# Kernel optimization log

Measured on AMD Instinct MI355X. Metric: run time of the kernel, lower is better.

Reference implementation:

```python
import jax, jax.numpy as jnp
import numpy as np

M, K, N = 8192, 4096, 4096
SCALE_D = 0.05  # per-tensor activation quant step

def setup_inputs() -> dict:
    key = jax.random.key(0)
    k1, k2, k3, k4 = jax.random.split(key, 4)
    x = jax.random.normal(k1, (M, K), jnp.float32)
    # already-quantized int8 weight, stored transposed as in the module: [K, N]
    q_weight = jax.random.randint(k2, (K, N), -127, 128).astype(jnp.int8)
    # per-tensor activation quant: act_scale = 1/scale_d, act_offset = 0
    act_scale = jnp.asarray(1.0 / SCALE_D, jnp.float32)
    act_offset = jnp.asarray(0.0, jnp.float32)
    # per-output-channel weight scales -> deq_scale = scale_d * scale_w, shape [N]
    scale_w = jax.random.uniform(k3, (N,), jnp.float32, 0.001, 0.01)
    deq_scale = (SCALE_D * scale_w).astype(jnp.float32)
    # int32 bias = round(bias_f / (scale_d * scale_w))
    bias_f = jax.random.normal(k4, (N,), jnp.float32) * 0.1
    bias_i32 = jnp.round(bias_f / deq_scale).astype(jnp.int32)
    return {"x": x, "q_weight": q_weight, "act_scale": act_scale,
            "act_offset": act_offset, "deq_scale": deq_scale, "bias_i32": bias_i32}

def reference(x, q_weight, act_scale, act_offset, deq_scale, bias_i32):
    # npu_quantize(div_mode=False): q = clamp(round(x * scale + offset), int8)
    qx = jnp.clip(jnp.round(x * act_scale + act_offset), -128.0, 127.0).astype(jnp.int8)
    # npu_quant_matmul: int8 GEMM accumulated in int32, + int32 bias, * deq_scale
    acc = jnp.matmul(qx.astype(jnp.int32), q_weight.astype(jnp.int32),
                     preferred_element_type=jnp.int32)  # [M, N] int32
    out = (acc + bias_i32[None, :]).astype(jnp.float32) * deq_scale[None, :]
    return out
```

## Files before the change

kernel.cpp:

```cpp
#include <hip/hip_runtime.h>
#include <stdint.h>

#define GM 8192
#define GK 4096
#define GN 4096

typedef int v4i __attribute__((ext_vector_type(4)));

__device__ __forceinline__ void async_load16(const void* gptr, void* lptr) {
  __builtin_amdgcn_global_load_lds(
      (const __attribute__((address_space(1))) void*)gptr,
      (__attribute__((address_space(3))) void*)lptr,
      16 , 0 , 0 );
}

__global__ __launch_bounds__(256) void quant_kernel(
    const float* __restrict__ x, int8_t* __restrict__ qx,
    const float* __restrict__ scale_p, const float* __restrict__ off_p) {
  const int i = blockIdx.x * 256 + threadIdx.x;
  const float s = scale_p[0], o = off_p[0];
  const float4 f = ((const float4*)x)[i];
  float a = fminf(fmaxf(rintf(f.x * s + o), -128.f), 127.f);
  float b = fminf(fmaxf(rintf(f.y * s + o), -128.f), 127.f);
  float c = fminf(fmaxf(rintf(f.z * s + o), -128.f), 127.f);
  float d = fminf(fmaxf(rintf(f.w * s + o), -128.f), 127.f);
  int packed = (((int)a) & 0xff) | ((((int)b) & 0xff) << 8) |
               ((((int)c) & 0xff) << 16) | ((((int)d) & 0xff) << 24);
  ((int*)qx)[i] = packed;
}

__global__ __launch_bounds__(256) void transpose_kernel(
    const int* __restrict__ B, int8_t* __restrict__ Bt) {
  __shared__ int tile32[64][65];
  const int t = threadIdx.x;
  const int n0 = blockIdx.x * 64;
  const int k0 = blockIdx.y * 64;
#pragma unroll
  for (int r = 0; r < 4; ++r) {
    const int kl = r * 16 + (t >> 4);
    const int nl = (t & 15) * 4;
    const int4 v = *(const int4*)(B + (size_t)(k0 + kl) * GN + n0 + nl);
    *(int4*)&tile32[kl][nl] = v;
  }
  __syncthreads();
  const int nl = t >> 2;
  const int kc = (t & 3) * 16;
  v4i out;
#pragma unroll
  for (int w = 0; w < 4; ++w) {
    int p = 0;
#pragma unroll
    for (int j = 0; j < 4; ++j)
      p |= (tile32[kc + w * 4 + j][nl] & 0xff) << (8 * j);
    out[w] = p;
  }
  *(v4i*)(Bt + (size_t)(n0 + nl) * GK + k0 + kc) = out;
}

__global__ __launch_bounds__(256) void gemm_i8_kernel(
    const int8_t* __restrict__ A, const int8_t* __restrict__ Bt,
    const int* __restrict__ bias, const float* __restrict__ deq,
    float* __restrict__ C) {
  __shared__ __align__(16) int8_t Alds[128 * 64];
  __shared__ __align__(16) int8_t Blds[128 * 64];

  const int t = threadIdx.x;
  const int lane = t & 63;
  const int wave = t >> 6;
  const int m0 = blockIdx.y * 128;
  const int n0 = blockIdx.x * 128;
  const int wm = (wave >> 1) * 64;
  const int wn = (wave & 1) * 64;

  v4i acc[4][4];
  const v4i vzero = {0, 0, 0, 0};
#pragma unroll
  for (int mi = 0; mi < 4; ++mi)
#pragma unroll
    for (int ni = 0; ni < 4; ++ni) acc[mi][ni] = vzero;

  const int srow = t >> 2;
  const int scol = (t & 3) * 16;
  const int8_t* ag0 = A + (size_t)(m0 + srow) * GK + scol;
  const int8_t* ag1 = ag0 + (size_t)64 * GK;
  const int8_t* bg0 = Bt + (size_t)(n0 + srow) * GK + scol;
  const int8_t* bg1 = bg0 + (size_t)64 * GK;
  int8_t* al0 = Alds + t * 16;
  int8_t* al1 = al0 + 64 * 64;
  int8_t* bl0 = Blds + t * 16;
  int8_t* bl1 = bl0 + 64 * 64;

  const int fr = lane & 15;
  const int kg = (lane >> 4) * 16;

  for (int k0 = 0; k0 < GK; k0 += 64) {
    __syncthreads();
    async_load16(ag0 + k0, al0);
    async_load16(ag1 + k0, al1);
    async_load16(bg0 + k0, bl0);
    async_load16(bg1 + k0, bl1);
    __syncthreads();

    v4i af[4], bf[4];
#pragma unroll
    for (int i = 0; i < 4; ++i) {
      af[i] = *(const v4i*)(Alds + (size_t)(wm + i * 16 + fr) * 64 + kg);
      bf[i] = *(const v4i*)(Blds + (size_t)(wn + i * 16 + fr) * 64 + kg);
    }
#pragma unroll
    for (int mi = 0; mi < 4; ++mi)
#pragma unroll
      for (int ni = 0; ni < 4; ++ni)
        acc[mi][ni] =
            __builtin_amdgcn_mfma_i32_16x16x64_i8(af[mi], bf[ni], acc[mi][ni], 0, 0, 0);
  }

  const int col = lane & 15;
  const int rq = (lane >> 4) * 4;
#pragma unroll
  for (int ni = 0; ni < 4; ++ni) {
    const int gc = n0 + wn + ni * 16 + col;
    const float d = deq[gc];
    const int bs = bias[gc];
#pragma unroll
    for (int mi = 0; mi < 4; ++mi) {
      const int gr = m0 + wm + mi * 16 + rq;
#pragma unroll
      for (int r = 0; r < 4; ++r)
        C[(size_t)(gr + r) * GN + gc] = (float)(acc[mi][ni][r] + bs) * d;
    }
  }
}

extern "C" void kernel_launch(void* const* d_in, const int* in_sizes, int n_in,
                              void* d_out, int out_size, void* d_ws, size_t ws_size,
                              hipStream_t stream) {
  const float* x = (const float*)d_in[0];
  const int* qw = (const int*)d_in[1];
  const float* act_scale = (const float*)d_in[2];
  const float* act_offset = (const float*)d_in[3];
  const float* deq = (const float*)d_in[4];
  const int* bias = (const int*)d_in[5];
  float* out = (float*)d_out;

  int8_t* qx = (int8_t*)d_ws;
  int8_t* Bt = (int8_t*)d_ws + (size_t)GM * GK;

  const int n4 = GM * GK / 4;
  quant_kernel<<<n4 / 256, 256, 0, stream>>>(x, qx, act_scale, act_offset);
  transpose_kernel<<<dim3(GN / 64, GK / 64), 256, 0, stream>>>(qw, Bt);
  gemm_i8_kernel<<<dim3(GN / 128, GM / 128), 256, 0, stream>>>(qx, Bt, bias, deq, out);
}
```

Before: 422.4 us.

## Fuse quant and transpose launches; process two K-tiles per barrier in int8 GEMM

Quantization and weight transpose are merged into one kernel launch, with block index selecting the job, which removes a launch and lets both jobs run concurrently. The GEMM main loop now loads two 64-wide K slices into two LDS buffers per iteration, halving the number of barrier pairs and increasing outstanding global loads. LDS use doubles to 32KB per block, which may reduce occupancy.

New measurement: 411.3 us. 2.6% less time.

```diff
diff --git a/kernel.cpp b/kernel.cpp
--- a/kernel.cpp
+++ b/kernel.cpp
@@ -14,55 +14,59 @@
       16 , 0 , 0 );
 }
 
-__global__ __launch_bounds__(256) void quant_kernel(
+#define TBLK ((GN / 64) * (GK / 64))
+#define QBLK (GM * GK / 4 / 256)
+
+__global__ __launch_bounds__(256) void prep_kernel(
     const float* __restrict__ x, int8_t* __restrict__ qx,
-    const float* __restrict__ scale_p, const float* __restrict__ off_p) {
-  const int i = blockIdx.x * 256 + threadIdx.x;
-  const float s = scale_p[0], o = off_p[0];
-  const float4 f = ((const float4*)x)[i];
-  float a = fminf(fmaxf(rintf(f.x * s + o), -128.f), 127.f);
-  float b = fminf(fmaxf(rintf(f.y * s + o), -128.f), 127.f);
-  float c = fminf(fmaxf(rintf(f.z * s + o), -128.f), 127.f);
-  float d = fminf(fmaxf(rintf(f.w * s + o), -128.f), 127.f);
-  int packed = (((int)a) & 0xff) | ((((int)b) & 0xff) << 8) |
-               ((((int)c) & 0xff) << 16) | ((((int)d) & 0xff) << 24);
-  ((int*)qx)[i] = packed;
-}
-
-__global__ __launch_bounds__(256) void transpose_kernel(
+    const float* __restrict__ scale_p, const float* __restrict__ off_p,
     const int* __restrict__ B, int8_t* __restrict__ Bt) {
   __shared__ int tile32[64][65];
+  const int b = blockIdx.x;
   const int t = threadIdx.x;
-  const int n0 = blockIdx.x * 64;
-  const int k0 = blockIdx.y * 64;
+  if (b < TBLK) {
+    const int n0 = (b & 63) * 64;
+    const int k0 = (b >> 6) * 64;
 #pragma unroll
-  for (int r = 0; r < 4; ++r) {
-    const int kl = r * 16 + (t >> 4);
-    const int nl = (t & 15) * 4;
-    const int4 v = *(const int4*)(B + (size_t)(k0 + kl) * GN + n0 + nl);
-    *(int4*)&tile32[kl][nl] = v;
+    for (int r = 0; r < 4; ++r) {
+      const int kl = r * 16 + (t >> 4);
+      const int nl = (t & 15) * 4;
+      const int4 v = *(const int4*)(B + (size_t)(k0 + kl) * GN + n0 + nl);
+      *(int4*)&tile32[kl][nl] = v;
+    }
+    __syncthreads();
+    const int nl = t >> 2;
+    const int kc = (t & 3) * 16;
+    v4i out;
+#pragma unroll
+    for (int w = 0; w < 4; ++w) {
+      int p = 0;
+#pragma unroll
+      for (int j = 0; j < 4; ++j)
+        p |= (tile32[kc + w * 4 + j][nl] & 0xff) << (8 * j);
+      out[w] = p;
+    }
+    *(v4i*)(Bt + (size_t)(n0 + nl) * GK + k0 + kc) = out;
+  } else {
+    const int i = (b - TBLK) * 256 + t;
+    const float s = scale_p[0], o = off_p[0];
+    const float4 f = ((const float4*)x)[i];
+    float a0 = fminf(fmaxf(rintf(f.x * s + o), -128.f), 127.f);
+    float b0 = fminf(fmaxf(rintf(f.y * s + o), -128.f), 127.f);
+    float c0 = fminf(fmaxf(rintf(f.z * s + o), -128.f), 127.f);
+    float d0 = fminf(fmaxf(rintf(f.w * s + o), -128.f), 127.f);
+    int packed = (((int)a0) & 0xff) | ((((int)b0) & 0xff) << 8) |
+                 ((((int)c0) & 0xff) << 16) | ((((int)d0) & 0xff) << 24);
+    ((int*)qx)[i] = packed;
   }
-  __syncthreads();
-  const int nl = t >> 2;
-  const int kc = (t & 3) * 16;
-  v4i out;
-#pragma unroll
-  for (int w = 0; w < 4; ++w) {
-    int p = 0;
-#pragma unroll
-    for (int j = 0; j < 4; ++j)
-      p |= (tile32[kc + w * 4 + j][nl] & 0xff) << (8 * j);
-    out[w] = p;
-  }
-  *(v4i*)(Bt + (size_t)(n0 + nl) * GK + k0 + kc) = out;
 }
 
 __global__ __launch_bounds__(256) void gemm_i8_kernel(
     const int8_t* __restrict__ A, const int8_t* __restrict__ Bt,
     const int* __restrict__ bias, const float* __restrict__ deq,
     float* __restrict__ C) {
-  __shared__ __align__(16) int8_t Alds[128 * 64];
-  __shared__ __align__(16) int8_t Blds[128 * 64];
+  __shared__ __align__(16) int8_t Alds[2][128 * 64];
+  __shared__ __align__(16) int8_t Blds[2][128 * 64];
 
   const int t = threadIdx.x;
   const int lane = t & 63;
@@ -81,38 +85,42 @@
 
   const int srow = t >> 2;
   const int scol = (t & 3) * 16;
-  const int8_t* ag0 = A + (size_t)(m0 + srow) * GK + scol;
-  const int8_t* ag1 = ag0 + (size_t)64 * GK;
-  const int8_t* bg0 = Bt + (size_t)(n0 + srow) * GK + scol;
-  const int8_t* bg1 = bg0 + (size_t)64 * GK;
-  int8_t* al0 = Alds + t * 16;
-  int8_t* al1 = al0 + 64 * 64;
-  int8_t* bl0 = Blds + t * 16;
-  int8_t* bl1 = bl0 + 64 * 64;
+  const int8_t* ag = A + (size_t)(m0 + srow) * GK + scol;
+  const int8_t* bg = Bt + (size_t)(n0 + srow) * GK + scol;
+  const size_t rg = (size_t)64 * GK;
+  int8_t* al = &Alds[0][0] + t * 16;
+  int8_t* bl = &Blds[0][0] + t * 16;
 
   const int fr = lane & 15;
   const int kg = (lane >> 4) * 16;
 
-  for (int k0 = 0; k0 < GK; k0 += 64) {
+  for (int k0 = 0; k0 < GK; k0 += 128) {
     __syncthreads();
-    async_load16(ag0 + k0, al0);
-    async_load16(ag1 + k0, al1);
-    async_load16(bg0 + k0, bl0);
-    async_load16(bg1 + k0, bl1);
+    async_load16(ag + k0, al);
+    async_load16(ag + rg + k0, al + 4096);
+    async_load16(bg + k0, bl);
+    async_load16(bg + rg + k0, bl + 4096);
+    async_load16(ag + k0 + 64, al + 8192);
+    async_load16(ag + rg + k0 + 64, al + 12288);
+    async_load16(bg + k0 + 64, bl + 8192);
+    async_load16(bg + rg + k0 + 64, bl + 12288);
     __syncthreads();
 
-    v4i af[4], bf[4];
 #pragma unroll
-    for (int i = 0; i < 4; ++i) {
-      af[i] = *(const v4i*)(Alds + (size_t)(wm + i * 16 + fr) * 64 + kg);
-      bf[i] = *(const v4i*)(Blds + (size_t)(wn + i * 16 + fr) * 64 + kg);
+    for (int s = 0; s < 2; ++s) {
+      v4i af[4], bf[4];
+#pragma unroll
+      for (int i = 0; i < 4; ++i) {
+        af[i] = *(const v4i*)(&Alds[s][0] + (size_t)(wm + i * 16 + fr) * 64 + kg);
+        bf[i] = *(const v4i*)(&Blds[s][0] + (size_t)(wn + i * 16 + fr) * 64 + kg);
+      }
+#pragma unroll
+      for (int mi = 0; mi < 4; ++mi)
+#pragma unroll
+        for (int ni = 0; ni < 4; ++ni)
+          acc[mi][ni] =
+              __builtin_amdgcn_mfma_i32_16x16x64_i8(af[mi], bf[ni], acc[mi][ni], 0, 0, 0);
     }
-#pragma unroll
-    for (int mi = 0; mi < 4; ++mi)
-#pragma unroll
-      for (int ni = 0; ni < 4; ++ni)
-        acc[mi][ni] =
-            __builtin_amdgcn_mfma_i32_16x16x64_i8(af[mi], bf[ni], acc[mi][ni], 0, 0, 0);
   }
 
   const int col = lane & 15;
@@ -146,8 +154,6 @@
   int8_t* qx = (int8_t*)d_ws;
   int8_t* Bt = (int8_t*)d_ws + (size_t)GM * GK;
 
-  const int n4 = GM * GK / 4;
-  quant_kernel<<<n4 / 256, 256, 0, stream>>>(x, qx, act_scale, act_offset);
-  transpose_kernel<<<dim3(GN / 64, GK / 64), 256, 0, stream>>>(qw, Bt);
+  prep_kernel<<<TBLK + QBLK, 256, 0, stream>>>(x, qx, act_scale, act_offset, qw, Bt);
   gemm_i8_kernel<<<dim3(GN / 128, GM / 128), 256, 0, stream>>>(qx, Bt, bias, deq, out);
 }
```
